# Kernel tuning notes

Hardware: AMD Instinct MI355X
Metric: run time of the kernel (lower is better)

## Reference

```python
import jax, jax.numpy as jnp
import numpy as np

B, N, D, K = 1024, 8192, 256, 8
LAMBDA_MULT = 0.01

def setup_inputs() -> dict:
    key = jax.random.key(0)
    k1, k2, k3, k4, k5 = jax.random.split(key, 5)
    x = jax.random.uniform(k1, (B, D), dtype=jnp.float32)
    mu = jax.random.uniform(k2, (N, D), dtype=jnp.float32)
    lambda_base = jax.random.uniform(k3, (N,), dtype=jnp.float32) * LAMBDA_MULT
    v = jax.random.normal(k4, (N, K, D), dtype=jnp.float32)  # stands in for per-unit orthogonal init
    omega = 0.1 + 0.4 * jax.random.uniform(k5, (N, K), dtype=jnp.float32)
    return {"x": x, "mu": mu, "lambda_base": lambda_base, "v": v, "omega": omega}

def reference(x, mu, lambda_base, v, omega):
    # quad_form = diff^T (lambda*I + sum_k omega_k v_k v_k^T) diff
    #           = lambda * ||x - mu||^2 + sum_k omega_k * ((x - mu) . v_k)^2
    # Woodbury-style expansion avoids materializing W:(n,d,d) and diff:(b,n,d).
    x2 = jnp.sum(x * x, axis=-1)                      # (b,)
    mu2 = jnp.sum(mu * mu, axis=-1)                   # (n,)
    xm = x @ mu.T                                     # (b,n)
    sqdist = x2[:, None] - 2.0 * xm + mu2[None, :]    # (b,n) = ||x-mu||^2
    xv = jnp.einsum('bd,nkd->bnk', x, v)              # (b,n,k)
    muv = jnp.einsum('nd,nkd->nk', mu, v)             # (n,k)
    proj2 = (xv - muv[None, :, :]) ** 2               # (b,n,k)
    quad = lambda_base[None, :] * sqdist + jnp.einsum('bnk,nk->bn', proj2, omega)
    return jnp.exp(-quad / D)  # Type == 'exp'
```

## Files before the change

kernel.cpp:

```cpp
#include <hip/hip_runtime.h>


#define B_SZ 1024
#define N_SZ 8192
#define D_SZ 256
#define K_SZ 8

#define BTM 256
#define BT 128
#define NT 16

typedef __bf16 bf16x8 __attribute__((ext_vector_type(8)));
typedef float f32x4 __attribute__((ext_vector_type(4)));
typedef unsigned short u16x4 __attribute__((ext_vector_type(4)));
typedef unsigned short u16x8 __attribute__((ext_vector_type(8)));

#define WS_X2   0u
#define WS_MU2  4096u
#define WS_MUV  36864u
#define WS_PX   299008u
#define WS_PW   823296u
#define WS_NEED (823296ull + 37748736ull)

__device__ __forceinline__ float wave_reduce(float s) {
#pragma unroll
  for (int off = 32; off > 0; off >>= 1) s += __shfl_down(s, off);
  return s;
}

__device__ __forceinline__ u16x4 cvt4(float4 t) {
  u16x4 r;
  r[0] = __builtin_bit_cast(unsigned short, (__bf16)t.x);
  r[1] = __builtin_bit_cast(unsigned short, (__bf16)t.y);
  r[2] = __builtin_bit_cast(unsigned short, (__bf16)t.z);
  r[3] = __builtin_bit_cast(unsigned short, (__bf16)t.w);
  return r;
}

__device__ __forceinline__ void glds16(const void* g, const void* l) {
  __builtin_amdgcn_global_load_lds(
      (const __attribute__((address_space(1))) void*)g,
      (__attribute__((address_space(3))) void*)l, 16, 0, 0);
}

__global__ void prep_all(const float* __restrict__ x, const float* __restrict__ mu,
                         const float* __restrict__ v,
                         float* __restrict__ x2, unsigned short* __restrict__ px,
                         float* __restrict__ mu2, float* __restrict__ muv,
                         unsigned short* __restrict__ pw) {
  const int w = threadIdx.x >> 6, lane = threadIdx.x & 63;
  const int g = blockIdx.x * 4 + w;
  if (g < B_SZ) {
    const int b = g;
    float4 t = *(const float4*)(x + (size_t)b * D_SZ + 4 * lane);
    *(u16x4*)(px + (size_t)b * D_SZ + 4 * lane) = cvt4(t);
    float s = t.x * t.x + t.y * t.y + t.z * t.z + t.w * t.w;
    s = wave_reduce(s);
    if (lane == 0) x2[b] = s;
  } else if (g < B_SZ + N_SZ) {
    const int n = g - B_SZ;
    float4 m4 = *(const float4*)(mu + (size_t)n * D_SZ + 4 * lane);
    *(u16x4*)(pw + (size_t)n * 9 * D_SZ + 4 * lane) = cvt4(m4);
    float s = m4.x * m4.x + m4.y * m4.y + m4.z * m4.z + m4.w * m4.w;
    s = wave_reduce(s);
    if (lane == 0) mu2[n] = s;
  } else {
    const int idx = g - (B_SZ + N_SZ);
    const int n = idx >> 3, k = idx & 7;
    float4 m4 = *(const float4*)(mu + (size_t)n * D_SZ + 4 * lane);
    float4 v4 = *(const float4*)(v + ((size_t)n * K_SZ + k) * D_SZ + 4 * lane);
    *(u16x4*)(pw + ((size_t)n * 9 + k + 1) * D_SZ + 4 * lane) = cvt4(v4);
    float s = m4.x * v4.x + m4.y * v4.y + m4.z * v4.z + m4.w * v4.w;
    s = wave_reduce(s);
    if (lane == 0) muv[n * K_SZ + k] = s;
  }
}

__device__ __forceinline__ void stage_tile(const unsigned short* __restrict__ px,
                                           const unsigned short* __restrict__ pw,
                                           unsigned short* As, unsigned short* Bs,
                                           int b0, int n0, int k0, int w, int lane) {
  const int nl4 = lane >> 2;
  const int ch = lane & 3;
  const int kc = (ch ^ ((nl4 >> 1) & 3)) * 8;
#pragma unroll
  for (int t = 0; t < 4; ++t) {
    int r0 = w * 64 + t * 16;
    glds16(px + (size_t)(b0 + r0 + nl4) * D_SZ + k0 + kc, As + r0 * 32);
  }
#pragma unroll
  for (int t = 0; t < 3; ++t) {
    int i = w + 4 * t;
    if (i < 9)
      glds16(pw + ((size_t)(n0 + nl4) * 9 + i) * D_SZ + k0 + kc, Bs + i * 16 * 32);
  }
}

__global__ __launch_bounds__(256, 2)
void hmu_main_p(const unsigned short* __restrict__ px,
                const unsigned short* __restrict__ pw,
                const float* __restrict__ lam, const float* __restrict__ om,
                const float* __restrict__ wsf, float* __restrict__ out) {
  __shared__ __align__(16) unsigned short As[BTM * 32];
  __shared__ __align__(16) unsigned short Bs[NT * 9 * 32];

  const float* ws_x2 = wsf;
  const float* ws_mu2 = wsf + 1024;
  const float* ws_muv = wsf + 9216;

  const int tid = threadIdx.x;
  const int lane = tid & 63;
  const int w = tid >> 6;
  const int m = lane & 15;
  const int kg = lane >> 4;

  const int bid = blockIdx.x;
  const int xcd = bid & 7;
  const int idx = bid >> 3;
  const int n0 = (xcd * 64 + (idx >> 2)) * NT;
  const int b0 = (idx & 3) * BTM;

  f32x4 acc[4][9];
#pragma unroll
  for (int rb = 0; rb < 4; ++rb)
#pragma unroll
    for (int j = 0; j < 9; ++j) acc[rb][j] = (f32x4){0.f, 0.f, 0.f, 0.f};

  const int sw = (kg ^ ((m >> 1) & 3)) * 8;

  for (int kt = 0; kt < 8; ++kt) {
    stage_tile(px, pw, As, Bs, b0, n0, kt * 32, w, lane);
    __syncthreads();

    bf16x8 bfr[9];
#pragma unroll
    for (int j = 0; j < 9; ++j)
      bfr[j] = *(const bf16x8*)&Bs[(j * 16 + m) * 32 + sw];
#pragma unroll
    for (int rb = 0; rb < 4; ++rb) {
      bf16x8 a = *(const bf16x8*)&As[((w * 4 + rb) * 16 + m) * 32 + sw];
#pragma unroll
      for (int j = 0; j < 9; ++j)
        acc[rb][j] = __builtin_amdgcn_mfma_f32_16x16x32_bf16(a, bfr[j], acc[rb][j], 0, 0, 0);
    }
    __syncthreads();
  }

  const int n = n0 + m;
  const float lam_n = lam[n];
  const float mu2_n = ws_mu2[n];
  float omr[8], muvr[8];
#pragma unroll
  for (int k = 0; k < 8; ++k) {
    omr[k] = om[n * 8 + k];
    muvr[k] = ws_muv[n * 8 + k];
  }
#pragma unroll
  for (int rb = 0; rb < 4; ++rb) {
#pragma unroll
    for (int r = 0; r < 4; ++r) {
      int b = b0 + (w * 4 + rb) * 16 + kg * 4 + r;
      float x2b = ws_x2[b];
      float c0 = acc[rb][0][r];
      float q = lam_n * (x2b - 2.f * c0 + mu2_n);
#pragma unroll
      for (int k = 0; k < 8; ++k) {
        float p = acc[rb][k + 1][r] - muvr[k];
        q = fmaf(omr[k] * p, p, q);
      }
      out[(size_t)b * N_SZ + n] = __expf(q * (-1.0f / 256.0f));
    }
  }
}

__device__ __forceinline__ void cvt16_store(const float* __restrict__ src,
                                            unsigned short* dst) {
  const float4* p4 = (const float4*)src;
  float fv[16];
#pragma unroll
  for (int e = 0; e < 4; ++e) {
    float4 t = p4[e];
    fv[4 * e + 0] = t.x; fv[4 * e + 1] = t.y;
    fv[4 * e + 2] = t.z; fv[4 * e + 3] = t.w;
  }
  u16x8 lo, hi;
#pragma unroll
  for (int e = 0; e < 8; ++e) {
    lo[e] = __builtin_bit_cast(unsigned short, (__bf16)fv[e]);
    hi[e] = __builtin_bit_cast(unsigned short, (__bf16)fv[e + 8]);
  }
  *(u16x8*)dst = lo;
  *(u16x8*)(dst + 8) = hi;
}

#define LDS_STRIDE 40
__global__ __launch_bounds__(256, 2)
void hmu_main_f(const float* __restrict__ x, const float* __restrict__ mu,
                const float* __restrict__ lam, const float* __restrict__ v,
                const float* __restrict__ om, const float* __restrict__ ws,
                float* __restrict__ out) {
  __shared__ __align__(16) unsigned short As[BT * LDS_STRIDE];
  __shared__ __align__(16) unsigned short Bs[NT * 9 * LDS_STRIDE];
  const float* ws_x2 = ws;
  const float* ws_mu2 = ws + 1024;
  const float* ws_muv = ws + 9216;
  const int tid = threadIdx.x, lane = tid & 63, w = tid >> 6;
  const int m = lane & 15, kg = lane >> 4;
  const int n0 = blockIdx.x * NT, b0 = blockIdx.y * BT;
  f32x4 acc[2][9];
#pragma unroll
  for (int bs = 0; bs < 2; ++bs)
#pragma unroll
    for (int j = 0; j < 9; ++j) acc[bs][j] = (f32x4){0.f, 0.f, 0.f, 0.f};
  const int arow = tid >> 1, ahalf = tid & 1;
  for (int kt = 0; kt < 8; ++kt) {
    const int k0 = kt * 32;
    cvt16_store(x + (size_t)(b0 + arow) * D_SZ + k0 + ahalf * 16,
                &As[arow * LDS_STRIDE + ahalf * 16]);
#pragma unroll
    for (int it = 0; it < 2; ++it) {
      int idx = tid + 256 * it;
      if (idx < 288) {
        int row = idx >> 1, half = idx & 1;
        int nl = row / 9, j = row - nl * 9;
        const float* src = (j == 0)
            ? mu + (size_t)(n0 + nl) * D_SZ + k0 + half * 16
            : v + (size_t)((n0 + nl) * K_SZ + (j - 1)) * D_SZ + k0 + half * 16;
        cvt16_store(src, &Bs[row * LDS_STRIDE + half * 16]);
      }
    }
    __syncthreads();
    bf16x8 af[2];
#pragma unroll
    for (int bs = 0; bs < 2; ++bs)
      af[bs] = *(const bf16x8*)&As[((2 * w + bs) * 16 + m) * LDS_STRIDE + kg * 8];
#pragma unroll
    for (int j = 0; j < 9; ++j) {
      bf16x8 bfr = *(const bf16x8*)&Bs[(m * 9 + j) * LDS_STRIDE + kg * 8];
      acc[0][j] = __builtin_amdgcn_mfma_f32_16x16x32_bf16(af[0], bfr, acc[0][j], 0, 0, 0);
      acc[1][j] = __builtin_amdgcn_mfma_f32_16x16x32_bf16(af[1], bfr, acc[1][j], 0, 0, 0);
    }
    __syncthreads();
  }
  const int n = n0 + m;
  const float lam_n = lam[n];
  const float mu2_n = ws_mu2[n];
  float omr[8], muvr[8];
#pragma unroll
  for (int k = 0; k < 8; ++k) {
    omr[k] = om[n * 8 + k];
    muvr[k] = ws_muv[n * 8 + k];
  }
#pragma unroll
  for (int bs = 0; bs < 2; ++bs)
#pragma unroll
    for (int r = 0; r < 4; ++r) {
      int b = b0 + (2 * w + bs) * 16 + kg * 4 + r;
      float c0 = acc[bs][0][r];
      float q = lam_n * (ws_x2[b] - 2.f * c0 + mu2_n);
#pragma unroll
      for (int k = 0; k < 8; ++k) {
        float p = acc[bs][k + 1][r] - muvr[k];
        q = fmaf(omr[k] * p, p, q);
      }
      out[(size_t)b * N_SZ + n] = __expf(q * (-1.0f / 256.0f));
    }
}

__global__ void p2_mu_f(const float* __restrict__ mu, const float* __restrict__ v,
                        float* __restrict__ mu2, float* __restrict__ muv) {
  __shared__ __align__(16) float mulds[D_SZ];
  const int n = blockIdx.x;
  const int w = threadIdx.x >> 6, lane = threadIdx.x & 63;
  if (w == 0) {
    float4 m4 = *(const float4*)(mu + (size_t)n * D_SZ + 4 * lane);
    *(float4*)(mulds + 4 * lane) = m4;
    float s = m4.x * m4.x + m4.y * m4.y + m4.z * m4.z + m4.w * m4.w;
    s = wave_reduce(s);
    if (lane == 0) mu2[n] = s;
  }
  __syncthreads();
  float4 m4 = *(const float4*)(mulds + 4 * lane);
#pragma unroll
  for (int kk = 0; kk < 2; ++kk) {
    const int k = w * 2 + kk;
    float4 v4 = *(const float4*)(v + ((size_t)n * K_SZ + k) * D_SZ + 4 * lane);
    float s = m4.x * v4.x + m4.y * v4.y + m4.z * v4.z + m4.w * v4.w;
    s = wave_reduce(s);
    if (lane == 0) muv[n * K_SZ + k] = s;
  }
}

__global__ void p1_x2_f(const float* __restrict__ x, float* __restrict__ x2) {
  const int w = threadIdx.x >> 6, lane = threadIdx.x & 63;
  const int b = blockIdx.x * 4 + w;
  float4 t = *(const float4*)(x + (size_t)b * D_SZ + 4 * lane);
  float s = t.x * t.x + t.y * t.y + t.z * t.z + t.w * t.w;
  s = wave_reduce(s);
  if (lane == 0) x2[b] = s;
}

extern "C" void kernel_launch(void* const* d_in, const int* in_sizes, int n_in,
                              void* d_out, int out_size, void* d_ws, size_t ws_size,
                              hipStream_t stream) {
  const float* x   = (const float*)d_in[0];
  const float* mu  = (const float*)d_in[1];
  const float* lam = (const float*)d_in[2];
  const float* v   = (const float*)d_in[3];
  const float* om  = (const float*)d_in[4];
  float* out = (float*)d_out;
  char* wsb = (char*)d_ws;
  float* wsf = (float*)d_ws;
  float* x2  = (float*)(wsb + WS_X2);
  float* mu2 = (float*)(wsb + WS_MU2);
  float* muv = (float*)(wsb + WS_MUV);

  if (ws_size >= WS_NEED) {
    unsigned short* px = (unsigned short*)(wsb + WS_PX);
    unsigned short* pw = (unsigned short*)(wsb + WS_PW);
    const int nunits = B_SZ + N_SZ + N_SZ * K_SZ;
    prep_all<<<nunits / 4, 256, 0, stream>>>(x, mu, v, x2, px, mu2, muv, pw);
    hmu_main_p<<<(N_SZ / NT) * (B_SZ / BTM), 256, 0, stream>>>(px, pw, lam, om, wsf, out);
  } else {
    dim3 grid(N_SZ / NT, B_SZ / BT);
    p1_x2_f<<<B_SZ / 4, 256, 0, stream>>>(x, x2);
    p2_mu_f<<<N_SZ, 256, 0, stream>>>(mu, v, mu2, muv);
    hmu_main_f<<<grid, 256, 0, stream>>>(x, mu, lam, v, om, wsf, out);
  }
}
```

Baseline: 162.3 us.

## Preload full B tile into LDS and stream A fragments from global with prefetch

The whole B panel (all 8 k-steps for 16 n-rows times 9 projections) is now staged into shared memory once up front, which removes the per-iteration __syncthreads pairs. The A operand skips LDS and is loaded straight from global into registers, with the next k-step prefetched in software. This cuts barrier stalls and LDS traffic, but uses more LDS (about 73KB) and more registers, and the A loads are direct global reads, which can hurt occupancy under launch_bounds(256,2).

```diff
diff --git a/kernel.cpp b/kernel.cpp
--- a/kernel.cpp
+++ b/kernel.cpp
@@ -76,33 +76,12 @@
   }
 }
 
-__device__ __forceinline__ void stage_tile(const unsigned short* __restrict__ px,
-                                           const unsigned short* __restrict__ pw,
-                                           unsigned short* As, unsigned short* Bs,
-                                           int b0, int n0, int k0, int w, int lane) {
-  const int nl4 = lane >> 2;
-  const int ch = lane & 3;
-  const int kc = (ch ^ ((nl4 >> 1) & 3)) * 8;
-#pragma unroll
-  for (int t = 0; t < 4; ++t) {
-    int r0 = w * 64 + t * 16;
-    glds16(px + (size_t)(b0 + r0 + nl4) * D_SZ + k0 + kc, As + r0 * 32);
-  }
-#pragma unroll
-  for (int t = 0; t < 3; ++t) {
-    int i = w + 4 * t;
-    if (i < 9)
-      glds16(pw + ((size_t)(n0 + nl4) * 9 + i) * D_SZ + k0 + kc, Bs + i * 16 * 32);
-  }
-}
-
 __global__ __launch_bounds__(256, 2)
 void hmu_main_p(const unsigned short* __restrict__ px,
                 const unsigned short* __restrict__ pw,
                 const float* __restrict__ lam, const float* __restrict__ om,
                 const float* __restrict__ wsf, float* __restrict__ out) {
-  __shared__ __align__(16) unsigned short As[BTM * 32];
-  __shared__ __align__(16) unsigned short Bs[NT * 9 * 32];
+  __shared__ __align__(16) unsigned short Bs[8 * 144 * 32];
 
   const float* ws_x2 = wsf;
   const float* ws_mu2 = wsf + 1024;
@@ -120,6 +99,26 @@
   const int n0 = (xcd * 64 + (idx >> 2)) * NT;
   const int b0 = (idx & 3) * BTM;
 
+  const unsigned short* pxw = px + (size_t)(b0 + w * 64 + m) * D_SZ + kg * 8;
+  bf16x8 a_nxt0 = *(const bf16x8*)(pxw + 0 * 16 * D_SZ);
+  bf16x8 a_nxt1 = *(const bf16x8*)(pxw + 1 * 16 * D_SZ);
+  bf16x8 a_nxt2 = *(const bf16x8*)(pxw + 2 * 16 * D_SZ);
+  bf16x8 a_nxt3 = *(const bf16x8*)(pxw + 3 * 16 * D_SZ);
+
+  {
+    const int nl4 = lane >> 2;
+    const int ch = lane & 3;
+    const int kc = (ch ^ ((nl4 >> 1) & 3)) * 8;
+#pragma unroll
+    for (int p = 0; p < 18; ++p) {
+      const int pair = w * 18 + p;
+      const int kt = pair / 9, j = pair % 9;
+      glds16(pw + ((size_t)(n0 + nl4) * 9 + j) * D_SZ + kt * 32 + kc,
+             Bs + (kt * 144 + j * 16) * 32);
+    }
+  }
+  __syncthreads();
+
   f32x4 acc[4][9];
 #pragma unroll
   for (int rb = 0; rb < 4; ++rb)
@@ -128,22 +127,23 @@
 
   const int sw = (kg ^ ((m >> 1) & 3)) * 8;
 
+#pragma unroll
   for (int kt = 0; kt < 8; ++kt) {
-    stage_tile(px, pw, As, Bs, b0, n0, kt * 32, w, lane);
-    __syncthreads();
-
-    bf16x8 bfr[9];
-#pragma unroll
-    for (int j = 0; j < 9; ++j)
-      bfr[j] = *(const bf16x8*)&Bs[(j * 16 + m) * 32 + sw];
-#pragma unroll
-    for (int rb = 0; rb < 4; ++rb) {
-      bf16x8 a = *(const bf16x8*)&As[((w * 4 + rb) * 16 + m) * 32 + sw];
-#pragma unroll
-      for (int j = 0; j < 9; ++j)
-        acc[rb][j] = __builtin_amdgcn_mfma_f32_16x16x32_bf16(a, bfr[j], acc[rb][j], 0, 0, 0);
-    }
-    __syncthreads();
+    bf16x8 a0 = a_nxt0, a1 = a_nxt1, a2 = a_nxt2, a3 = a_nxt3;
+    if (kt < 7) {
+      a_nxt0 = *(const bf16x8*)(pxw + 0 * 16 * D_SZ + (kt + 1) * 32);
+      a_nxt1 = *(const bf16x8*)(pxw + 1 * 16 * D_SZ + (kt + 1) * 32);
+      a_nxt2 = *(const bf16x8*)(pxw + 2 * 16 * D_SZ + (kt + 1) * 32);
+      a_nxt3 = *(const bf16x8*)(pxw + 3 * 16 * D_SZ + (kt + 1) * 32);
+    }
+#pragma unroll
+    for (int j = 0; j < 9; ++j) {
+      bf16x8 bfr = *(const bf16x8*)&Bs[(kt * 144 + j * 16 + m) * 32 + sw];
+      acc[0][j] = __builtin_amdgcn_mfma_f32_16x16x32_bf16(a0, bfr, acc[0][j], 0, 0, 0);
+      acc[1][j] = __builtin_amdgcn_mfma_f32_16x16x32_bf16(a1, bfr, acc[1][j], 0, 0, 0);
+      acc[2][j] = __builtin_amdgcn_mfma_f32_16x16x32_bf16(a2, bfr, acc[2][j], 0, 0, 0);
+      acc[3][j] = __builtin_amdgcn_mfma_f32_16x16x32_bf16(a3, bfr, acc[3][j], 0, 0, 0);
+    }
   }
 
   const int n = n0 + m;
```

New measurement: 169.7 us. 1.05x slower.

## Split projection columns across waves with register-resident weights and LDS reduction

Applied to the files above, without the earlier changes.

Replaces the LDS-staged GEMM main kernel with one where each wave keeps its share of the nine 16-column weight slices (mu plus eight v's) for a 16-unit tile in registers for the whole K loop. It streams bf16 x rows directly from global memory, and partial quadratic terms from the four waves are summed through a small LDS scratch before the exp and a vectorized output store. Each block now covers 512 batch rows instead of 256. The aim is to drop the per-k-tile global-to-LDS staging and barriers and to write output in 16-byte chunks. The cost is imbalanced MFMA work (wave 0 does three slices, the others two), redundant global reads of x by every wave, and two barriers per group of tiles.

```diff
diff --git a/kernel.cpp b/kernel.cpp
--- a/kernel.cpp
+++ b/kernel.cpp
@@ -6,7 +6,6 @@
 #define D_SZ 256
 #define K_SZ 8
 
-#define BTM 256
 #define BT 128
 #define NT 16
 
@@ -35,12 +34,6 @@
   r[2] = __builtin_bit_cast(unsigned short, (__bf16)t.z);
   r[3] = __builtin_bit_cast(unsigned short, (__bf16)t.w);
   return r;
-}
-
-__device__ __forceinline__ void glds16(const void* g, const void* l) {
-  __builtin_amdgcn_global_load_lds(
-      (const __attribute__((address_space(1))) void*)g,
-      (__attribute__((address_space(3))) void*)l, 16, 0, 0);
 }
 
 __global__ void prep_all(const float* __restrict__ x, const float* __restrict__ mu,
@@ -76,33 +69,12 @@
   }
 }
 
-__device__ __forceinline__ void stage_tile(const unsigned short* __restrict__ px,
-                                           const unsigned short* __restrict__ pw,
-                                           unsigned short* As, unsigned short* Bs,
-                                           int b0, int n0, int k0, int w, int lane) {
-  const int nl4 = lane >> 2;
-  const int ch = lane & 3;
-  const int kc = (ch ^ ((nl4 >> 1) & 3)) * 8;
-#pragma unroll
-  for (int t = 0; t < 4; ++t) {
-    int r0 = w * 64 + t * 16;
-    glds16(px + (size_t)(b0 + r0 + nl4) * D_SZ + k0 + kc, As + r0 * 32);
-  }
-#pragma unroll
-  for (int t = 0; t < 3; ++t) {
-    int i = w + 4 * t;
-    if (i < 9)
-      glds16(pw + ((size_t)(n0 + nl4) * 9 + i) * D_SZ + k0 + kc, Bs + i * 16 * 32);
-  }
-}
-
 __global__ __launch_bounds__(256, 2)
-void hmu_main_p(const unsigned short* __restrict__ px,
-                const unsigned short* __restrict__ pw,
-                const float* __restrict__ lam, const float* __restrict__ om,
-                const float* __restrict__ wsf, float* __restrict__ out) {
-  __shared__ __align__(16) unsigned short As[BTM * 32];
-  __shared__ __align__(16) unsigned short Bs[NT * 9 * 32];
+void hmu_ws(const unsigned short* __restrict__ px,
+            const unsigned short* __restrict__ pw,
+            const float* __restrict__ lam, const float* __restrict__ om,
+            const float* __restrict__ wsf, float* __restrict__ out) {
+  __shared__ __align__(16) float scr[4 * 4 * 16 * 16];
 
   const float* ws_x2 = wsf;
   const float* ws_mu2 = wsf + 1024;
@@ -111,65 +83,108 @@
   const int tid = threadIdx.x;
   const int lane = tid & 63;
   const int w = tid >> 6;
-  const int m = lane & 15;
+  const int c = lane & 15;
   const int kg = lane >> 4;
 
   const int bid = blockIdx.x;
   const int xcd = bid & 7;
   const int idx = bid >> 3;
-  const int n0 = (xcd * 64 + (idx >> 2)) * NT;
-  const int b0 = (idx & 3) * BTM;
-
-  f32x4 acc[4][9];
-#pragma unroll
-  for (int rb = 0; rb < 4; ++rb)
-#pragma unroll
-    for (int j = 0; j < 9; ++j) acc[rb][j] = (f32x4){0.f, 0.f, 0.f, 0.f};
-
-  const int sw = (kg ^ ((m >> 1) & 3)) * 8;
-
-  for (int kt = 0; kt < 8; ++kt) {
-    stage_tile(px, pw, As, Bs, b0, n0, kt * 32, w, lane);
+  const int n0 = (xcd * 64 + (idx >> 1)) * NT;
+  const int bs = idx & 1;
+
+  const int wsel = (w + bid) & 3;
+  const int jbase = (wsel == 0) ? 0 : (2 * wsel + 1);
+  const int jcnt = (wsel == 0) ? 3 : 2;
+
+  const int kpair = (wsel == 0) ? 0 : 2 * wsel;
+  float lamr[4], lm2r[4], omA[4], omB[4], muvA[4], muvB[4];
+#pragma unroll
+  for (int r = 0; r < 4; ++r) {
+    int n_r = n0 + kg * 4 + r;
+    if (wsel == 0) {
+      lamr[r] = lam[n_r];
+      lm2r[r] = ws_mu2[n_r];
+    }
+    omA[r] = om[n_r * 8 + kpair];
+    omB[r] = om[n_r * 8 + kpair + 1];
+    muvA[r] = ws_muv[n_r * 8 + kpair];
+    muvB[r] = ws_muv[n_r * 8 + kpair + 1];
+  }
+
+  bf16x8 wf[3][8];
+#pragma unroll
+  for (int jj = 0; jj < 3; ++jj) {
+    if (jj < jcnt) {
+#pragma unroll
+      for (int kt = 0; kt < 8; ++kt)
+        wf[jj][kt] = *(const bf16x8*)(
+            pw + ((size_t)(n0 + c) * 9 + (jbase + jj)) * D_SZ + kt * 32 + kg * 8);
+    }
+  }
+
+  const unsigned short* pxb = px + (size_t)(bs * 512 + c) * D_SZ + kg * 8;
+
+  for (int g = 0; g < 8; ++g) {
+#pragma unroll
+    for (int t = 0; t < 4; ++t) {
+      const int tile = g * 4 + t;
+      const unsigned short* pxt = pxb + (size_t)tile * 16 * D_SZ;
+
+      f32x4 acc0 = (f32x4){0.f, 0.f, 0.f, 0.f};
+      f32x4 acc1 = (f32x4){0.f, 0.f, 0.f, 0.f};
+      f32x4 acc2 = (f32x4){0.f, 0.f, 0.f, 0.f};
+
+      bf16x8 xf[2];
+      xf[0] = *(const bf16x8*)(pxt);
+      xf[1] = *(const bf16x8*)(pxt + 32);
+#pragma unroll
+      for (int kt = 0; kt < 8; ++kt) {
+        bf16x8 xc = xf[kt & 1];
+        if (kt < 6) xf[kt & 1] = *(const bf16x8*)(pxt + (kt + 2) * 32);
+        acc0 = __builtin_amdgcn_mfma_f32_16x16x32_bf16(wf[0][kt], xc, acc0, 0, 0, 0);
+        acc1 = __builtin_amdgcn_mfma_f32_16x16x32_bf16(wf[1][kt], xc, acc1, 0, 0, 0);
+        if (wsel == 0)
+          acc2 = __builtin_amdgcn_mfma_f32_16x16x32_bf16(wf[2][kt], xc, acc2, 0, 0, 0);
+      }
+
+      f32x4 qv;
+      if (wsel == 0) {
+        float x2b = ws_x2[bs * 512 + tile * 16 + c];
+#pragma unroll
+        for (int r = 0; r < 4; ++r) {
+          float q = lamr[r] * (x2b - 2.f * acc0[r] + lm2r[r]);
+          float pA = acc1[r] - muvA[r];
+          q = fmaf(omA[r] * pA, pA, q);
+          float pB = acc2[r] - muvB[r];
+          qv[r] = fmaf(omB[r] * pB, pB, q);
+        }
+      } else {
+#pragma unroll
+        for (int r = 0; r < 4; ++r) {
+          float pA = acc0[r] - muvA[r];
+          float q = omA[r] * pA * pA;
+          float pB = acc1[r] - muvB[r];
+          qv[r] = fmaf(omB[r] * pB, pB, q);
+        }
+      }
+      *(f32x4*)&scr[((t * 4 + wsel) * 16 + c) * 16 + kg * 4] = qv;
+    }
     __syncthreads();
 
-    bf16x8 bfr[9];
-#pragma unroll
-    for (int j = 0; j < 9; ++j)
-      bfr[j] = *(const bf16x8*)&Bs[(j * 16 + m) * 32 + sw];
-#pragma unroll
-    for (int rb = 0; rb < 4; ++rb) {
-      bf16x8 a = *(const bf16x8*)&As[((w * 4 + rb) * 16 + m) * 32 + sw];
-#pragma unroll
-      for (int j = 0; j < 9; ++j)
-        acc[rb][j] = __builtin_amdgcn_mfma_f32_16x16x32_bf16(a, bfr[j], acc[rb][j], 0, 0, 0);
+    {
+      f32x4 s0 = *(const f32x4*)&scr[((w * 4 + 0) * 16 + c) * 16 + kg * 4];
+      f32x4 s1 = *(const f32x4*)&scr[((w * 4 + 1) * 16 + c) * 16 + kg * 4];
+      f32x4 s2 = *(const f32x4*)&scr[((w * 4 + 2) * 16 + c) * 16 + kg * 4];
+      f32x4 s3 = *(const f32x4*)&scr[((w * 4 + 3) * 16 + c) * 16 + kg * 4];
+      f32x4 o;
+#pragma unroll
+      for (int r = 0; r < 4; ++r) {
+        float q = (s0[r] + s1[r]) + (s2[r] + s3[r]);
+        o[r] = __expf(q * (-1.0f / 256.0f));
+      }
+      *(f32x4*)(out + (size_t)(bs * 512 + (g * 4 + w) * 16 + c) * N_SZ + n0 + kg * 4) = o;
     }
     __syncthreads();
-  }
-
-  const int n = n0 + m;
-  const float lam_n = lam[n];
-  const float mu2_n = ws_mu2[n];
-  float omr[8], muvr[8];
-#pragma unroll
-  for (int k = 0; k < 8; ++k) {
-    omr[k] = om[n * 8 + k];
-    muvr[k] = ws_muv[n * 8 + k];
-  }
-#pragma unroll
-  for (int rb = 0; rb < 4; ++rb) {
-#pragma unroll
-    for (int r = 0; r < 4; ++r) {
-      int b = b0 + (w * 4 + rb) * 16 + kg * 4 + r;
-      float x2b = ws_x2[b];
-      float c0 = acc[rb][0][r];
-      float q = lam_n * (x2b - 2.f * c0 + mu2_n);
-#pragma unroll
-      for (int k = 0; k < 8; ++k) {
-        float p = acc[rb][k + 1][r] - muvr[k];
-        q = fmaf(omr[k] * p, p, q);
-      }
-      out[(size_t)b * N_SZ + n] = __expf(q * (-1.0f / 256.0f));
-    }
   }
 }
 
@@ -320,7 +335,7 @@
     unsigned short* pw = (unsigned short*)(wsb + WS_PW);
     const int nunits = B_SZ + N_SZ + N_SZ * K_SZ;
     prep_all<<<nunits / 4, 256, 0, stream>>>(x, mu, v, x2, px, mu2, muv, pw);
-    hmu_main_p<<<(N_SZ / NT) * (B_SZ / BTM), 256, 0, stream>>>(px, pw, lam, om, wsf, out);
+    hmu_ws<<<1024, 256, 0, stream>>>(px, pw, lam, om, wsf, out);
   } else {
     dim3 grid(N_SZ / NT, B_SZ / BT);
     p1_x2_f<<<B_SZ / 4, 256, 0, stream>>>(x, x2);
```

Result: slower. 310.4 us (+91.3%).

## Double-buffer LDS tiles to overlap global-to-LDS loads with MFMA

Applied to the files above, without the earlier changes.

Splits the A and B shared-memory tiles into two buffers and prefetches the next K-slice while the current one is computed. Explicit vmcnt waits, sized to each wave's number of outstanding loads, replace the full syncthreads, and s_setprio raises priority around the MFMA block. This is meant to hide global-load latency behind compute. In exchange it doubles LDS use, which may cut occupancy, and the hand-counted vmcnt values are fragile if the load count per wave changes.

```diff
diff --git a/kernel.cpp b/kernel.cpp
--- a/kernel.cpp
+++ b/kernel.cpp
@@ -101,8 +101,8 @@
                 const unsigned short* __restrict__ pw,
                 const float* __restrict__ lam, const float* __restrict__ om,
                 const float* __restrict__ wsf, float* __restrict__ out) {
-  __shared__ __align__(16) unsigned short As[BTM * 32];
-  __shared__ __align__(16) unsigned short Bs[NT * 9 * 32];
+  __shared__ __align__(16) unsigned short As[2][BTM * 32];
+  __shared__ __align__(16) unsigned short Bs[2][NT * 9 * 32];
 
   const float* ws_x2 = wsf;
   const float* ws_mu2 = wsf + 1024;
@@ -128,22 +128,39 @@
 
   const int sw = (kg ^ ((m >> 1) & 3)) * 8;
 
+  stage_tile(px, pw, As[0], Bs[0], b0, n0, 0, w, lane);
+
+#pragma unroll
   for (int kt = 0; kt < 8; ++kt) {
-    stage_tile(px, pw, As, Bs, b0, n0, kt * 32, w, lane);
-    __syncthreads();
-
+    const int cur = kt & 1;
+    if (kt < 7) {
+      stage_tile(px, pw, As[cur ^ 1], Bs[cur ^ 1], b0, n0, (kt + 1) * 32, w, lane);
+      if (w == 0) asm volatile("s_waitcnt vmcnt(7)" ::: "memory");
+      else        asm volatile("s_waitcnt vmcnt(6)" ::: "memory");
+    } else {
+      asm volatile("s_waitcnt vmcnt(0)" ::: "memory");
+    }
+    __builtin_amdgcn_s_barrier();
+
+    const unsigned short* Ac = As[cur];
+    const unsigned short* Bc = Bs[cur];
     bf16x8 bfr[9];
 #pragma unroll
     for (int j = 0; j < 9; ++j)
-      bfr[j] = *(const bf16x8*)&Bs[(j * 16 + m) * 32 + sw];
+      bfr[j] = *(const bf16x8*)&Bc[(j * 16 + m) * 32 + sw];
+    __builtin_amdgcn_s_setprio(1);
 #pragma unroll
     for (int rb = 0; rb < 4; ++rb) {
-      bf16x8 a = *(const bf16x8*)&As[((w * 4 + rb) * 16 + m) * 32 + sw];
+      bf16x8 a = *(const bf16x8*)&Ac[((w * 4 + rb) * 16 + m) * 32 + sw];
 #pragma unroll
       for (int j = 0; j < 9; ++j)
         acc[rb][j] = __builtin_amdgcn_mfma_f32_16x16x32_bf16(a, bfr[j], acc[rb][j], 0, 0, 0);
     }
-    __syncthreads();
+    __builtin_amdgcn_s_setprio(0);
+    if (kt < 7) {
+      asm volatile("s_waitcnt lgkmcnt(0)" ::: "memory");
+      __builtin_amdgcn_s_barrier();
+    }
   }
 
   const int n = n0 + m;
```

New measurement: 161.6 us. No clear change (-0.4%).
